# Performance work log

Hardware: AMD Instinct MI355X
Metric: run time of the kernel (lower is better)

Reference implementation:

```python
import jax, jax.numpy as jnp
import numpy as np
from jax import lax


def _conv(x, w, b):
    y = lax.conv_general_dilated(x, w, window_strides=(1, 1), padding='SAME',
                                 dimension_numbers=('NCHW', 'OIHW', 'NCHW'))
    return y + b[None, :, None, None]


def _maxpool2(x):
    return lax.reduce_window(x, -jnp.inf, lax.max,
                             window_dimensions=(1, 1, 2, 2),
                             window_strides=(1, 1, 2, 2), padding='VALID')


def setup_inputs() -> dict:
    key = jax.random.key(0)
    ks = jax.random.split(key, 11)
    f32 = jnp.float32
    return {
        'x': jax.random.normal(ks[0], (512, 1, 112, 112), f32),
        'w_conv1': jax.random.normal(ks[1], (8, 1, 3, 3), f32) * 0.1,
        'b_conv1': jax.random.normal(ks[2], (8,), f32) * 0.1,
        'w_conv2': jax.random.normal(ks[3], (16, 8, 3, 3), f32) * 0.1,
        'b_conv2': jax.random.normal(ks[4], (16,), f32) * 0.1,
        'w_patch': jax.random.normal(ks[5], (4, 64), f32) * 0.1,
        'b_patch': jax.random.normal(ks[6], (4,), f32) * 0.1,
        'w_fc1': jax.random.normal(ks[7], (64, 784), f32) * 0.05,
        'b_fc1': jax.random.normal(ks[8], (64,), f32) * 0.05,
        'w_fc2': jax.random.normal(ks[9], (10, 64), f32) * 0.05,
        'b_fc2': jax.random.normal(ks[10], (10,), f32) * 0.05,
    }


def reference(x, w_conv1, b_conv1, w_conv2, b_conv2, w_patch, b_patch,
              w_fc1, b_fc1, w_fc2, b_fc2):
    B = x.shape[0]
    h = _maxpool2(jax.nn.relu(_conv(x, w_conv1, b_conv1)))        # [B,8,56,56]
    f = _maxpool2(jax.nn.relu(_conv(h, w_conv2, b_conv2)))        # [B,16,28,28]
    C, H, W = f.shape[1], f.shape[2], f.shape[3]
    # im2col: 2x2 non-overlapping spatial patches, flattened as (C,2,2) -> 64
    p = f.reshape(B, C, H // 2, 2, W // 2, 2)
    p = p.transpose(0, 2, 4, 1, 3, 5).reshape(B, (H // 2) * (W // 2), C * 4)  # [B,196,64]
    pf = jnp.einsum('bpk,ok->bpo', p, w_patch) + b_patch          # [B,196,4]
    pf = pf.reshape(B, -1)                                        # [B,784]
    h1 = jax.nn.relu(pf @ w_fc1.T + b_fc1)
    logits = h1 @ w_fc2.T + b_fc2
    return jax.nn.log_softmax(logits, axis=-1)
```

## Files before the change

kernel.cpp:

```cpp
#include <hip/hip_runtime.h>


#define HS 58
#define FS 72
#define FSW 36

typedef _Float16 half2_t __attribute__((ext_vector_type(2)));
typedef _Float16 f16x8 __attribute__((ext_vector_type(8)));
typedef float f32x4 __attribute__((ext_vector_type(4)));
typedef float f32x2 __attribute__((ext_vector_type(2)));
typedef float f32x4u __attribute__((ext_vector_type(4), aligned(4)));

__device__ __forceinline__ unsigned pack_f16(float a, float b) {
  union { half2_t h; unsigned u; } z;
  z.h[0] = (_Float16)a;
  z.h[1] = (_Float16)b;
  return z.u;
}

__device__ __forceinline__ f16x8 as_f16x8(uint4 u) {
  union { uint4 u; f16x8 f; } z;
  z.u = u;
  return z.f;
}

__global__ __launch_bounds__(1024, 8) void k_all(
    const float* __restrict__ x, const float* __restrict__ w1,
    const float* __restrict__ b1, const float* __restrict__ w2,
    const float* __restrict__ b2, const float* __restrict__ wp,
    const float* __restrict__ bp, const float* __restrict__ w_fc1,
    const float* __restrict__ b_fc1, const float* __restrict__ w_fc2,
    const float* __restrict__ b_fc2, float* __restrict__ out) {
  __shared__ __align__(16) unsigned hsu[HS * HS * 4];
  __shared__ __align__(16) unsigned bwl[768];
  __shared__ __align__(16) unsigned fsu[122 * FSW];
  __shared__ __align__(16) float pfl[784];
  __shared__ float h1s[64];
  const int tid = threadIdx.x;
  const int b = blockIdx.x;
  const int l = tid & 63;
  const int wv = __builtin_amdgcn_readfirstlane(tid >> 6);
  const float* xb = x + (long)b * 12544;

  if (tid < 228) {
    int i = tid, hr, hc;
    if (i < 58) { hr = 0; hc = i; }
    else if (i < 116) { hr = 57; hc = i - 58; }
    else if (i < 172) { hr = i - 115; hc = 0; }
    else { hr = i - 171; hc = 57; }
    *(uint4*)(hsu + (hr * HS + hc) * 4) = make_uint4(0u, 0u, 0u, 0u);
  }
  if (tid < 768) {
    int t = tid, oc = t / 48, rem = t - oc * 48;
    int tap = rem >> 2, w = rem & 3;
    unsigned v = 0u;
    if (tap < 9)
      v = pack_f16(w2[(oc * 8 + 2 * w) * 9 + tap],
                   w2[(oc * 8 + 2 * w + 1) * 9 + tap]);
    bwl[t] = v;
  }

  for (int task = tid; task < 3136; task += 1024) {
    int gr = task / 56, gc = task - gr * 56;
    float win[4][4];
    int iy0 = 2 * gr - 1, ix0 = 2 * gc - 1;
    if (gr >= 1 && gr <= 54 && gc >= 1 && gc <= 54) {
      const float* xp = xb + iy0 * 112 + ix0;
#pragma unroll
      for (int rr = 0; rr < 4; ++rr) {
        f32x4u v = *(const f32x4u*)(xp + rr * 112);
        win[rr][0] = v.x; win[rr][1] = v.y; win[rr][2] = v.z; win[rr][3] = v.w;
      }
    } else {
#pragma unroll
      for (int rr = 0; rr < 4; ++rr) {
        int iy = iy0 + rr;
        bool yok = (unsigned)iy < 112u;
#pragma unroll
        for (int qq = 0; qq < 4; ++qq) {
          int ix = ix0 + qq;
          win[rr][qq] = (yok && (unsigned)ix < 112u) ? xb[iy * 112 + ix] : 0.f;
        }
      }
    }
    float hv[8];
#pragma unroll
    for (int ch = 0; ch < 8; ++ch) {
      f32x2 sA = {0.f, 0.f};
      f32x2 sB = {0.f, 0.f};
#pragma unroll
      for (int ty = 0; ty < 3; ++ty)
#pragma unroll
        for (int tx = 0; tx < 3; ++tx) {
          float wk = w1[ch * 9 + ty * 3 + tx];
          f32x2 wkk = {wk, wk};
          f32x2 xa = {win[ty][tx], win[ty][tx + 1]};
          f32x2 xb2 = {win[ty + 1][tx], win[ty + 1][tx + 1]};
          sA = __builtin_elementwise_fma(xa, wkk, sA);
          sB = __builtin_elementwise_fma(xb2, wkk, sB);
        }
      f32x2 sm = __builtin_elementwise_max(sA, sB);
      float m = fmaxf(sm.x, sm.y);
      hv[ch] = fmaxf(m + b1[ch], 0.f);
    }
    uint4 hw;
    hw.x = pack_f16(hv[0], hv[1]);
    hw.y = pack_f16(hv[2], hv[3]);
    hw.z = pack_f16(hv[4], hv[5]);
    hw.w = pack_f16(hv[6], hv[7]);
    *(uint4*)(hsu + ((gr + 1) * HS + gc + 1) * 4) = hw;
  }
  __syncthreads();

  {
    const int q = l >> 4;
    const int oc = l & 15;
    const int yoff = 2 * ((l >> 3) & 1) + ((l >> 1) & 1);
    const int xoff = 2 * ((l >> 2) & 1) + (l & 1);
    int poff[3];
#pragma unroll
    for (int kk = 0; kk < 3; ++kk) {
      int t = kk * 4 + q;
      int tt = t < 9 ? t : 8;
      int ty = tt / 3, tx = tt - ty * 3;
      poff[kk] = ((yoff + ty) * HS + xoff + tx) * 4;
    }
    uint4 bu0 = *(const uint4*)(bwl + (oc * 12 + 0 + q) * 4);
    uint4 bu1 = *(const uint4*)(bwl + (oc * 12 + 4 + q) * 4);
    uint4 bu2 = *(const uint4*)(bwl + (oc * 12 + 8 + q) * 4);
    const float b2v = b2[oc];

    f16x8 wpf0 = {}, wpf1 = {};
    float bpj = 0.f;
    if (oc < 4) {
      const float* wr = wp + oc * 64 + q * 8;
      float4 wa = *(const float4*)(wr);
      float4 wb = *(const float4*)(wr + 4);
      float4 wc = *(const float4*)(wr + 32);
      float4 wd = *(const float4*)(wr + 36);
      union { unsigned u[4]; f16x8 v; } u0, u1;
      u0.u[0] = pack_f16(wa.x, wa.y);
      u0.u[1] = pack_f16(wa.z, wa.w);
      u0.u[2] = pack_f16(wb.x, wb.y);
      u0.u[3] = pack_f16(wb.z, wb.w);
      u1.u[0] = pack_f16(wc.x, wc.y);
      u1.u[1] = pack_f16(wc.z, wc.w);
      u1.u[2] = pack_f16(wd.x, wd.y);
      u1.u[3] = pack_f16(wd.z, wd.w);
      wpf0 = u0.v;
      wpf1 = u1.v;
      bpj = bp[oc];
    }

    _Float16* fsh = (_Float16*)fsu;
    const int NP = (wv < 4) ? 13 : 12;
    const int G0 = (wv < 4) ? 13 * wv : 12 * wv + 4;
    const int RW = 7 * wv;
    const int npA = (NP + 1) >> 1;

    for (int hlf = 0; hlf < 2; ++hlf) {
      const int np = hlf ? NP - npA : npA;
      const int g0 = hlf ? G0 + npA : G0;
      for (int i = 0; i < np; ++i) {
        int p = g0 + i;
        int py = p / 14, px = p - py * 14;
        int pb = (4 * py * HS + 4 * px) * 4;
        uint4 a0u = *(const uint4*)(hsu + pb + poff[0]);
        uint4 a1u = *(const uint4*)(hsu + pb + poff[1]);
        uint4 a2u = *(const uint4*)(hsu + pb + poff[2]);
        f32x4 acc = {0.f, 0.f, 0.f, 0.f};
        acc = __builtin_amdgcn_mfma_f32_16x16x32_f16(as_f16x8(a0u), as_f16x8(bu0), acc, 0, 0, 0);
        acc = __builtin_amdgcn_mfma_f32_16x16x32_f16(as_f16x8(a1u), as_f16x8(bu1), acc, 0, 0, 0);
        acc = __builtin_amdgcn_mfma_f32_16x16x32_f16(as_f16x8(a2u), as_f16x8(bu2), acc, 0, 0, 0);
        float mx = fmaxf(fmaxf(acc[0], acc[1]), fmaxf(acc[2], acc[3]));
        float fv = fmaxf(mx + b2v, 0.f);
        fsh[(RW + i) * FS + oc * 4 + q] = (_Float16)fv;
      }
      asm volatile("s_waitcnt lgkmcnt(0)" ::: "memory");
      __builtin_amdgcn_sched_barrier(0);
      const unsigned* ar = fsu + (RW + oc) * FSW + q * 4;
      uint4 pa0 = *(const uint4*)(ar);
      uint4 pa1 = *(const uint4*)(ar + 16);
      f32x4 pc = {0.f, 0.f, 0.f, 0.f};
      pc = __builtin_amdgcn_mfma_f32_16x16x32_f16(as_f16x8(pa0), wpf0, pc, 0, 0, 0);
      pc = __builtin_amdgcn_mfma_f32_16x16x32_f16(as_f16x8(pa1), wpf1, pc, 0, 0, 0);
      if (oc < 4) {
#pragma unroll
        for (int i2 = 0; i2 < 4; ++i2) {
          int prow = q * 4 + i2;
          if (prow < np) pfl[(g0 + prow) * 4 + oc] = pc[i2] + bpj;
        }
      }
      asm volatile("" ::: "memory");
    }
  }
  __syncthreads();

  {
    int j = tid >> 4, q16 = tid & 15;
    const float* wrow = w_fc1 + j * 784;
    float acc = 0.f;
    for (int lp = q16; lp < 196; lp += 16) {
      float4 w4 = *(const float4*)(wrow + lp * 4);
      float4 p4 = *(const float4*)(pfl + lp * 4);
      acc += w4.x * p4.x + w4.y * p4.y + w4.z * p4.z + w4.w * p4.w;
    }
    acc += __shfl_down(acc, 8, 16);
    acc += __shfl_down(acc, 4, 16);
    acc += __shfl_down(acc, 2, 16);
    acc += __shfl_down(acc, 1, 16);
    if (q16 == 0) h1s[j] = fmaxf(acc + b_fc1[j], 0.f);
  }
  __syncthreads();

  if (wv == 0) {
    float h = h1s[l];
    float lg[10];
#pragma unroll
    for (int o = 0; o < 10; ++o) {
      float t = h * w_fc2[o * 64 + l];
#pragma unroll
      for (int off = 32; off; off >>= 1) t += __shfl_xor(t, off);
      lg[o] = t + b_fc2[o];
    }
    float mx = lg[0];
#pragma unroll
    for (int o = 1; o < 10; ++o) mx = fmaxf(mx, lg[o]);
    float se = 0.f;
#pragma unroll
    for (int o = 0; o < 10; ++o) se += __expf(lg[o] - mx);
    float ls = mx + __logf(se);
#pragma unroll
    for (int o = 0; o < 10; ++o)
      if (l == o) out[b * 10 + o] = lg[o] - ls;
  }
}

extern "C" void kernel_launch(void* const* d_in, const int* in_sizes, int n_in,
                              void* d_out, int out_size, void* d_ws, size_t ws_size,
                              hipStream_t stream) {
  const float* x = (const float*)d_in[0];
  const float* w1 = (const float*)d_in[1];
  const float* b1 = (const float*)d_in[2];
  const float* w2 = (const float*)d_in[3];
  const float* b2 = (const float*)d_in[4];
  const float* wp = (const float*)d_in[5];
  const float* bp = (const float*)d_in[6];
  const float* wf1 = (const float*)d_in[7];
  const float* bf1 = (const float*)d_in[8];
  const float* wf2 = (const float*)d_in[9];
  const float* bf2 = (const float*)d_in[10];
  (void)d_ws; (void)ws_size;

  k_all<<<dim3(512), 1024, 0, stream>>>(x, w1, b1, w2, b2, wp, bp, wf1, bf1,
                                        wf2, bf2, (float*)d_out);
}
```

Baseline: 116.1 us.

## Use fp16 dot2 for conv1 and split interior/border work

Conv1 now converts input pixel pairs to fp16 and uses v_dot2 instructions against packed fp16 weights held in shared memory, with the third tap kept in fp32 FMA. Interior tiles take a branch-free vectorized load path, and border tiles are handled by a separate group of threads with bounds checks. An extra __syncthreads is added so the packed weights are ready before use. This trades some conv1 input precision (round-toward-zero fp16) for fewer VALU instructions and less divergence.

```diff
diff --git a/kernel.cpp b/kernel.cpp
--- a/kernel.cpp
+++ b/kernel.cpp
@@ -6,9 +6,9 @@
 #define FSW 36
 
 typedef _Float16 half2_t __attribute__((ext_vector_type(2)));
+typedef __fp16 fp16r2 __attribute__((ext_vector_type(2)));
 typedef _Float16 f16x8 __attribute__((ext_vector_type(8)));
 typedef float f32x4 __attribute__((ext_vector_type(4)));
-typedef float f32x2 __attribute__((ext_vector_type(2)));
 typedef float f32x4u __attribute__((ext_vector_type(4), aligned(4)));
 
 __device__ __forceinline__ unsigned pack_f16(float a, float b) {
@@ -18,10 +18,69 @@
   return z.u;
 }
 
+__device__ __forceinline__ half2_t pkrtz2(float a, float b) {
+#if __has_builtin(__builtin_amdgcn_cvt_pkrtz)
+  union { fp16r2 r; half2_t h; } z;
+  z.r = __builtin_amdgcn_cvt_pkrtz(a, b);
+  return z.h;
+#else
+  half2_t h;
+  h[0] = (_Float16)a;
+  h[1] = (_Float16)b;
+  return h;
+#endif
+}
+
+__device__ __forceinline__ half2_t as_h2(unsigned u) {
+  union { unsigned u; half2_t h; } z;
+  z.u = u;
+  return z.h;
+}
+
 __device__ __forceinline__ f16x8 as_f16x8(uint4 u) {
   union { uint4 u; f16x8 f; } z;
   z.u = u;
   return z.f;
+}
+
+__device__ __forceinline__ float fdot2_(half2_t a, half2_t b, float c) {
+#if __has_builtin(__builtin_amdgcn_fdot2)
+  return __builtin_amdgcn_fdot2(a, b, c, false);
+#else
+  return c + (float)a[0] * (float)b[0] + (float)a[1] * (float)b[1];
+#endif
+}
+
+__device__ __forceinline__ void conv8(const float win[4][4],
+                                      const unsigned* wpl,
+                                      const float* __restrict__ w1,
+                                      const float* __restrict__ b1,
+                                      float hv[8]) {
+  half2_t p0[4], p1[4];
+#pragma unroll
+  for (int r = 0; r < 4; ++r) {
+    p0[r] = pkrtz2(win[r][0], win[r][1]);
+    p1[r] = pkrtz2(win[r][1], win[r][2]);
+  }
+#pragma unroll
+  for (int ch = 0; ch < 8; ++ch) {
+    float s00 = 0.f, s01 = 0.f, s10 = 0.f, s11 = 0.f;
+#pragma unroll
+    for (int t = 0; t < 3; ++t) {
+      half2_t w01 = as_h2(wpl[ch * 3 + t]);
+      float w2 = w1[ch * 9 + t * 3 + 2];
+      s00 = fdot2_(p0[t], w01, s00);
+      s00 = __builtin_fmaf(w2, win[t][2], s00);
+      s01 = fdot2_(p1[t], w01, s01);
+      s01 = __builtin_fmaf(w2, win[t][3], s01);
+      s10 = fdot2_(p0[t + 1], w01, s10);
+      s10 = __builtin_fmaf(w2, win[t + 1][2], s10);
+      s11 = fdot2_(p1[t + 1], w01, s11);
+      s11 = __builtin_fmaf(w2, win[t + 1][3], s11);
+    }
+    float m = fmaxf(fmaxf(s00, s01), fmaxf(s10, s11));
+    hv[ch] = fmaxf(m + b1[ch], 0.f);
+  }
 }
 
 __global__ __launch_bounds__(1024, 8) void k_all(
@@ -33,6 +92,7 @@
     const float* __restrict__ b_fc2, float* __restrict__ out) {
   __shared__ __align__(16) unsigned hsu[HS * HS * 4];
   __shared__ __align__(16) unsigned bwl[768];
+  __shared__ __align__(16) unsigned wpl[24];
   __shared__ __align__(16) unsigned fsu[122 * FSW];
   __shared__ __align__(16) float pfl[784];
   __shared__ float h1s[64];
@@ -59,50 +119,52 @@
                    w2[(oc * 8 + 2 * w + 1) * 9 + tap]);
     bwl[t] = v;
   }
-
-  for (int task = tid; task < 3136; task += 1024) {
-    int gr = task / 56, gc = task - gr * 56;
+  if (tid >= 768 && tid < 792) {
+    int t2 = tid - 768;
+    int ch = t2 / 3, t = t2 - ch * 3;
+    wpl[t2] = pack_f16(w1[ch * 9 + t * 3], w1[ch * 9 + t * 3 + 1]);
+  }
+  __syncthreads();
+
+  for (int t = tid; t < 2916; t += 1024) {
+    int gr = 1 + t / 54, gc = 1 + t % 54;
+    const float* xp = xb + (2 * gr - 1) * 112 + (2 * gc - 1);
     float win[4][4];
+#pragma unroll
+    for (int rr = 0; rr < 4; ++rr) {
+      f32x4u v = *(const f32x4u*)(xp + rr * 112);
+      win[rr][0] = v.x; win[rr][1] = v.y; win[rr][2] = v.z; win[rr][3] = v.w;
+    }
+    float hv[8];
+    conv8(win, wpl, w1, b1, hv);
+    uint4 hw;
+    hw.x = pack_f16(hv[0], hv[1]);
+    hw.y = pack_f16(hv[2], hv[3]);
+    hw.z = pack_f16(hv[4], hv[5]);
+    hw.w = pack_f16(hv[6], hv[7]);
+    *(uint4*)(hsu + ((gr + 1) * HS + gc + 1) * 4) = hw;
+  }
+  if (tid >= 804) {
+    int i = tid - 804;
+    int gr, gc;
+    if (i < 56) { gr = 0; gc = i; }
+    else if (i < 112) { gr = 55; gc = i - 56; }
+    else if (i < 166) { gr = i - 111; gc = 0; }
+    else { gr = i - 165; gc = 55; }
     int iy0 = 2 * gr - 1, ix0 = 2 * gc - 1;
-    if (gr >= 1 && gr <= 54 && gc >= 1 && gc <= 54) {
-      const float* xp = xb + iy0 * 112 + ix0;
-#pragma unroll
-      for (int rr = 0; rr < 4; ++rr) {
-        f32x4u v = *(const f32x4u*)(xp + rr * 112);
-        win[rr][0] = v.x; win[rr][1] = v.y; win[rr][2] = v.z; win[rr][3] = v.w;
+    float win[4][4];
+#pragma unroll
+    for (int rr = 0; rr < 4; ++rr) {
+      int iy = iy0 + rr;
+      bool yok = (unsigned)iy < 112u;
+#pragma unroll
+      for (int qq = 0; qq < 4; ++qq) {
+        int ix = ix0 + qq;
+        win[rr][qq] = (yok && (unsigned)ix < 112u) ? xb[iy * 112 + ix] : 0.f;
       }
-    } else {
-#pragma unroll
-      for (int rr = 0; rr < 4; ++rr) {
-        int iy = iy0 + rr;
-        bool yok = (unsigned)iy < 112u;
-#pragma unroll
-        for (int qq = 0; qq < 4; ++qq) {
-          int ix = ix0 + qq;
-          win[rr][qq] = (yok && (unsigned)ix < 112u) ? xb[iy * 112 + ix] : 0.f;
-        }
-      }
     }
     float hv[8];
-#pragma unroll
-    for (int ch = 0; ch < 8; ++ch) {
-      f32x2 sA = {0.f, 0.f};
-      f32x2 sB = {0.f, 0.f};
-#pragma unroll
-      for (int ty = 0; ty < 3; ++ty)
-#pragma unroll
-        for (int tx = 0; tx < 3; ++tx) {
-          float wk = w1[ch * 9 + ty * 3 + tx];
-          f32x2 wkk = {wk, wk};
-          f32x2 xa = {win[ty][tx], win[ty][tx + 1]};
-          f32x2 xb2 = {win[ty + 1][tx], win[ty + 1][tx + 1]};
-          sA = __builtin_elementwise_fma(xa, wkk, sA);
-          sB = __builtin_elementwise_fma(xb2, wkk, sB);
-        }
-      f32x2 sm = __builtin_elementwise_max(sA, sB);
-      float m = fmaxf(sm.x, sm.y);
-      hv[ch] = fmaxf(m + b1[ch], 0.f);
-    }
+    conv8(win, wpl, w1, b1, hv);
     uint4 hw;
     hw.x = pack_f16(hv[0], hv[1]);
     hw.y = pack_f16(hv[2], hv[3]);
```

New measurement: 111.0 us. 4.3% less time.
